# Optimization experiments

Measured on AMD Instinct MI355X. Metric: run time of the kernel, lower is better.

The kernel has to match this reference:

```python
import jax, jax.numpy as jnp
import numpy as np

N, D = 2, 256
M, L, K, DV = 8, 4, 4, 32
LK = L * K
LEVEL_HW = [(96, 96), (48, 48), (24, 24), (12, 12)]
S = sum(h * w for h, w in LEVEL_HW)  # 12240 flattened pyramid tokens
Q = S
OFFSET_SCALE = 0.5  # sampling_offset_scale_factor


def setup_inputs() -> dict:
    ks = jax.random.split(jax.random.key(0), 16)
    def lin(k, din, dout):
        return jax.random.normal(k, (din, dout), jnp.float32) / np.sqrt(din)
    return {
        "queries": jax.random.normal(ks[0], (N, Q, D), jnp.float32),
        "query_geometries": jax.random.uniform(ks[1], (N, Q, 4), jnp.float32, minval=0.1, maxval=0.9),
        "src_values": jax.random.normal(ks[2], (N, S, D), jnp.float32),
        "W_off": lin(ks[3], D, M * LK * 2) * 0.01,
        "b_off": jax.random.normal(ks[4], (M * LK * 2,), jnp.float32),
        "W_attn": lin(ks[5], D, M * LK),
        "b_attn": jnp.zeros((M * LK,), jnp.float32),
        "W_val": lin(ks[6], D, M * DV),
        "b_val": jnp.zeros((M * DV,), jnp.float32),
        "W_out": lin(ks[7], M * DV, D),
        "b_out": jnp.zeros((D,), jnp.float32),
    }


def _bilinear_sample(vmap_l, grid):
    # vmap_l: [B, dv, H, W]; grid: [B, Q, K, 2] in [-1, 1]
    # Matches F.grid_sample(mode='bilinear', align_corners=False, padding_mode='zeros')
    B, dv, H, W = vmap_l.shape
    x = (grid[..., 0] + 1.0) * (W / 2) - 0.5
    y = (grid[..., 1] + 1.0) * (H / 2) - 0.5
    x0 = jnp.floor(x)
    y0 = jnp.floor(y)
    wx = x - x0
    wy = y - y0
    x0i = x0.astype(jnp.int32)
    y0i = y0.astype(jnp.int32)
    vflat = vmap_l.reshape(B, dv, H * W)

    def corner(xi, yi, w):
        valid = (xi >= 0) & (xi < W) & (yi >= 0) & (yi < H)
        idx = jnp.clip(yi, 0, H - 1) * W + jnp.clip(xi, 0, W - 1)
        g = jax.vmap(lambda vf, i: vf[:, i])(vflat, idx)  # [B, dv, Q, K]
        return g * (w * valid)[:, None, :, :]

    return (corner(x0i, y0i, (1 - wx) * (1 - wy))
            + corner(x0i + 1, y0i, wx * (1 - wy))
            + corner(x0i, y0i + 1, (1 - wx) * wy)
            + corner(x0i + 1, y0i + 1, wx * wy))


def msdeform(queries, query_geometries, src_values, W_off, b_off, W_attn, b_attn,
             W_val, b_val, W_out, b_out):
    # attention weights: softmax over the L*K samples of each head
    attn = jax.nn.softmax((queries @ W_attn + b_attn).reshape(N, Q, M, LK), axis=-1)
    # predicted sampling offsets [N, Q, M, LK, 2]
    off = (queries @ W_off + b_off).reshape(N, Q, M, LK, 2)
    xy = query_geometries[..., :2]
    wh = query_geometries[..., 2:]
    scale = wh * (OFFSET_SCALE / K)  # wh * kv_count_per_level_inverse * sampling_offset_max_value
    pos = xy[:, :, None, None, :] + off * scale[:, :, None, None, :]  # normalized [0,1]
    # collapse (batch, head) -> B = N*M, rescale to [-1,1] for grid_sample semantics
    grid = (2.0 * pos - 1.0).transpose(0, 2, 1, 3, 4).reshape(N * M, Q, LK, 2)
    # project values and rebuild the per-level feature maps
    v = (src_values @ W_val + b_val).reshape(N, S, M, DV)
    samples, s = [], 0
    for l, (H, W) in enumerate(LEVEL_HW):
        vl = v[:, s:s + H * W].reshape(N, H, W, M, DV).transpose(0, 3, 4, 1, 2).reshape(N * M, DV, H, W)
        samples.append(_bilinear_sample(vl, grid[:, :, l * K:(l + 1) * K]))  # [N*M, DV, Q, K]
        s += H * W
    sampled = jnp.concatenate(samples, axis=-1)  # [N*M, DV, Q, LK]
    aw = attn.transpose(0, 2, 1, 3).reshape(N * M, 1, Q, LK)
    out = (sampled * aw).sum(-1)  # weighted reduction -> [N*M, DV, Q]
    out = out.reshape(N, M, DV, Q).transpose(0, 3, 1, 2).reshape(N, Q, M * DV)
    return out @ W_out + b_out  # backprojector


def reference(queries, query_geometries, src_values, W_off, b_off, W_attn, b_attn,
              W_val, b_val, W_out, b_out):
    return msdeform(queries, query_geometries, src_values, W_off, b_off, W_attn,
                    b_attn, W_val, b_val, W_out, b_out)
```

## Files before the change

kernel.cpp:

```cpp
#include <hip/hip_runtime.h>
#include <hip/hip_bf16.h>
#include <hip/hip_fp16.h>
#include <cstddef>

#define NB 2
#define QN 12240
#define SN 12240
#define MREAL 24480
#define MPAD  24576
#define MT    192

typedef unsigned short ushortT;
typedef unsigned int uintT;
typedef __bf16 bf16x8 __attribute__((ext_vector_type(8)));
typedef float f32x4 __attribute__((ext_vector_type(4)));
typedef float f32x2 __attribute__((ext_vector_type(2)));

__device__ __forceinline__ ushortT f2bf(float f) {
    uintT u = __float_as_uint(f);
    uintT r = u + 0x7fffu + ((u >> 16) & 1u);
    return (ushortT)(r >> 16);
}
__device__ __forceinline__ float bf_lo(uintT u) {
    return __uint_as_float(u << 16);
}
__device__ __forceinline__ float bf_hi(uintT u) {
    return __uint_as_float(u & 0xffff0000u);
}

__device__ __forceinline__ void async_ld16(const ushortT* g, ushortT* l) {
    __builtin_amdgcn_global_load_lds(
        (const __attribute__((address_space(1))) unsigned int*)g,
        (__attribute__((address_space(3))) unsigned int*)l, 16, 0, 0);
}

__global__ __launch_bounds__(256) void cast_all(
    const float* __restrict__ q, const float* __restrict__ src,
    const float* __restrict__ Wval, const float* __restrict__ Wattn,
    const float* __restrict__ Woff, const float* __restrict__ Wout,
    ushortT* __restrict__ qb, ushortT* __restrict__ sb,
    ushortT* __restrict__ tval, ushortT* __restrict__ tlo,
    ushortT* __restrict__ tout)
{
    int bx = blockIdx.x;
    if (bx < 6120) {
        const int issrc = bx >= 3060;
        const size_t idx = ((size_t)(bx - (issrc ? 3060 : 0)) * 256 + threadIdx.x) * 8;
        const float* in = issrc ? src : q;
        ushortT* out = issrc ? sb : qb;
        const float4 a = *(const float4*)(in + idx);
        const float4 b = *(const float4*)(in + idx + 4);
        uint4 o;
        o.x = (uintT)f2bf(a.x) | ((uintT)f2bf(a.y) << 16);
        o.y = (uintT)f2bf(a.z) | ((uintT)f2bf(a.w) << 16);
        o.z = (uintT)f2bf(b.x) | ((uintT)f2bf(b.y) << 16);
        o.w = (uintT)f2bf(b.z) | ((uintT)f2bf(b.w) << 16);
        *(uint4*)(out + idx) = o;
        return;
    }
    bx -= 6120;
    const float* W; ushortT* T; int n, Nw, trow;
    if (bx < 256)      { W = Wval;  T = tval; n = bx;       Nw = 256; trow = n; }
    else if (bx < 384) { W = Wattn; T = tlo;  n = bx - 256; Nw = 128; trow = n; }
    else if (bx < 640) { W = Woff;  T = tlo;  n = bx - 384; Nw = 256; trow = n + 128; }
    else               { W = Wout;  T = tout; n = bx - 640; Nw = 256; trow = n; }
    const int k = threadIdx.x;
    T[(size_t)trow * 256 + k] = f2bf(W[(size_t)k * Nw + n]);
}

__global__ __launch_bounds__(256) void gemm_vlo(
    const ushortT* __restrict__ q_bf, const ushortT* __restrict__ src_bf,
    const ushortT* __restrict__ wt_val, const ushortT* __restrict__ wt_lo,
    const float* __restrict__ b_val, const float* __restrict__ b_attn,
    const float* __restrict__ b_off,
    ushortT* __restrict__ v_bf, float* __restrict__ lo_ws)
{
    const int z = blockIdx.x >= 2;
    const int col0 = (z ? blockIdx.x - 2 : blockIdx.x) * 128;

    __shared__ __attribute__((aligned(16))) ushortT As[128 * 32];
    __shared__ __attribute__((aligned(16))) ushortT Bs[128 * 32];

    const ushortT* A  = z ? q_bf : src_bf;
    const ushortT* Bt = z ? wt_lo : wt_val;

    const int tid  = threadIdx.x;
    const int wave = tid >> 6;
    const int lane = tid & 63;
    const int row0 = blockIdx.y * 128;
    const int wr = (wave >> 1) * 64;
    const int wc = (wave & 1) * 64;

    f32x4 acc[4][4];
    #pragma unroll
    for (int i = 0; i < 4; i++)
        #pragma unroll
        for (int j = 0; j < 4; j++)
            acc[i][j] = (f32x4)0.f;

    const int srow = (lane >> 2);
    const int sk8  = (lane & 3) * 8;

    for (int k0 = 0; k0 < 256; k0 += 32) {
        #pragma unroll
        for (int j = 0; j < 2; j++) {
            const int r = wave * 32 + j * 16;
            async_ld16(A  + (size_t)(row0 + r + srow) * 256 + k0 + sk8, &As[r * 32]);
            async_ld16(Bt + (size_t)(col0 + r + srow) * 256 + k0 + sk8, &Bs[r * 32]);
        }
        __syncthreads();

        bf16x8 af[4], bfr[4];
        const int mrow = lane & 15;
        const int kq   = (lane >> 4) * 8;
        #pragma unroll
        for (int i = 0; i < 4; i++) {
            af[i]  = *(const bf16x8*)&As[(wr + i * 16 + mrow) * 32 + kq];
            bfr[i] = *(const bf16x8*)&Bs[(wc + i * 16 + mrow) * 32 + kq];
        }
        #pragma unroll
        for (int i = 0; i < 4; i++)
            #pragma unroll
            for (int j = 0; j < 4; j++)
                acc[i][j] = __builtin_amdgcn_mfma_f32_16x16x32_bf16(
                    af[i], bfr[j], acc[i][j], 0, 0, 0);
        __syncthreads();
    }

    const float* bp = z ? ((col0 < 128) ? b_attn : b_off) : b_val;
    const int cofs  = (z && col0 >= 128) ? 128 : 0;

    #pragma unroll
    for (int i = 0; i < 4; i++) {
        const int rbase = row0 + wr + i * 16 + ((lane >> 4) << 2);
        #pragma unroll
        for (int j = 0; j < 4; j++) {
            const int col = col0 + wc + j * 16 + (lane & 15);
            const float bb = bp[col - cofs];
            #pragma unroll
            for (int r = 0; r < 4; r++) {
                const int row = rbase + r;
                if (row < MREAL) {
                    const float val = acc[i][j][r] + bb;
                    if (z) {
                        lo_ws[(size_t)row * 384 + col] = val;
                    } else {
                        const int nn = row / SN;
                        const int s  = row - nn * SN;
                        const int head = col >> 5, ch = col & 31;
                        v_bf[(((size_t)nn * 8 + head) * SN + s) * 32 + ch] = f2bf(val);
                    }
                }
            }
        }
    }
}

__global__ __launch_bounds__(256) void gemm_out(
    const ushortT* __restrict__ A, const ushortT* __restrict__ Bt,
    const float* __restrict__ bias, float* __restrict__ C)
{
    __shared__ __attribute__((aligned(16))) ushortT As[128 * 32];
    __shared__ __attribute__((aligned(16))) ushortT Bs[128 * 32];

    const int tid  = threadIdx.x;
    const int wave = tid >> 6;
    const int lane = tid & 63;
    const int row0 = blockIdx.y * 128;
    const int col0 = blockIdx.x * 128;
    const int wr = (wave >> 1) * 64;
    const int wc = (wave & 1) * 64;

    f32x4 acc[4][4];
    #pragma unroll
    for (int i = 0; i < 4; i++)
        #pragma unroll
        for (int j = 0; j < 4; j++)
            acc[i][j] = (f32x4)0.f;

    const int srow = (lane >> 2);
    const int sk8  = (lane & 3) * 8;

    for (int k0 = 0; k0 < 256; k0 += 32) {
        #pragma unroll
        for (int j = 0; j < 2; j++) {
            const int r = wave * 32 + j * 16;
            async_ld16(A  + (size_t)(row0 + r + srow) * 256 + k0 + sk8, &As[r * 32]);
            async_ld16(Bt + (size_t)(col0 + r + srow) * 256 + k0 + sk8, &Bs[r * 32]);
        }
        __syncthreads();

        bf16x8 af[4], bfr[4];
        const int mrow = lane & 15;
        const int kq   = (lane >> 4) * 8;
        #pragma unroll
        for (int i = 0; i < 4; i++) {
            af[i]  = *(const bf16x8*)&As[(wr + i * 16 + mrow) * 32 + kq];
            bfr[i] = *(const bf16x8*)&Bs[(wc + i * 16 + mrow) * 32 + kq];
        }
        #pragma unroll
        for (int i = 0; i < 4; i++)
            #pragma unroll
            for (int j = 0; j < 4; j++)
                acc[i][j] = __builtin_amdgcn_mfma_f32_16x16x32_bf16(
                    af[i], bfr[j], acc[i][j], 0, 0, 0);
        __syncthreads();
    }

    #pragma unroll
    for (int i = 0; i < 4; i++) {
        const int rbase = row0 + wr + i * 16 + ((lane >> 4) << 2);
        #pragma unroll
        for (int j = 0; j < 4; j++) {
            const int col = col0 + wc + j * 16 + (lane & 15);
            const float bb = bias[col];
            #pragma unroll
            for (int r = 0; r < 4; r++) {
                const int row = rbase + r;
                if (row < MREAL)
                    C[(size_t)row * 256 + col] = acc[i][j][r] + bb;
            }
        }
    }
}

__global__ __launch_bounds__(128) void sample_kernel(
    const float* __restrict__ lo,
    const float* __restrict__ geom,
    const ushortT* __restrict__ v,
    ushortT* __restrict__ out)
{
    const int tid  = threadIdx.x;
    const int w    = tid >> 6;
    const int lane = tid & 63;
    const int qi   = lane >> 3;
    const int m    = blockIdx.y;
    const int n    = blockIdx.z;
    const int q    = blockIdx.x * 16 + w * 8 + qi;

    __shared__ __attribute__((aligned(16))) int pls[2][1568];

    const size_t qb = (size_t)n * QN + q;

    {
        const int p = lane & 7;
        const float* lorow = lo + qb * 384;
        const float2 lg = *(const float2*)(lorow + m * 16 + p * 2);
        const float4 of = *(const float4*)(lorow + 128 + m * 32 + p * 4);
        const float4 g  = *(const float4*)(geom + qb * 4);

        float mx = fmaxf(lg.x, lg.y);
        mx = fmaxf(mx, __shfl_xor(mx, 1));
        mx = fmaxf(mx, __shfl_xor(mx, 2));
        mx = fmaxf(mx, __shfl_xor(mx, 4));
        const float e0 = __expf(lg.x - mx);
        const float e1 = __expf(lg.y - mx);
        float s = e0 + e1;
        s += __shfl_xor(s, 1);
        s += __shfl_xor(s, 2);
        s += __shfl_xor(s, 4);
        const float inv = 1.f / s;

        const int l  = p >> 1;
        const int Wl = 96 >> l;
        const int s0 = (l == 0) ? 0 : (l == 1) ? 9216 : (l == 2) ? 11520 : 12096;
        const float cx = g.x, cy = g.y;
        const float sx = g.z * 0.125f, sy = g.w * 0.125f;
        int* myrec = &pls[w][qi * 196 + p * 24];

        #pragma unroll
        for (int t = 0; t < 2; t++) {
            const float ox = t ? of.z : of.x;
            const float oy = t ? of.w : of.y;
            const float wa = (t ? e1 : e0) * inv;

            const float x = (cx + ox * sx) * (float)Wl - 0.5f;
            const float y = (cy + oy * sy) * (float)Wl - 0.5f;
            const float xf = floorf(x), yf = floorf(y);
            const int x0 = (int)xf, y0 = (int)yf;
            const float wx = x - xf, wy = y - yf;

            const bool vx0 = (x0 >= 0) & (x0 < Wl);
            const bool vx1 = (x0 + 1 >= 0) & (x0 + 1 < Wl);
            const bool vy0 = (y0 >= 0) & (y0 < Wl);
            const bool vy1 = (y0 + 1 >= 0) & (y0 + 1 < Wl);

            const float w00 = (vx0 & vy0) ? wa * (1.f - wx) * (1.f - wy) : 0.f;
            const float w10 = (vx1 & vy0) ? wa * wx * (1.f - wy) : 0.f;
            const float w01 = (vx0 & vy1) ? wa * (1.f - wx) * wy : 0.f;
            const float w11 = (vx1 & vy1) ? wa * wx * wy : 0.f;

            const int xc0 = min(max(x0, 0), Wl - 1);
            const int xc1 = min(max(x0 + 1, 0), Wl - 1);
            const int yc0 = min(max(y0, 0), Wl - 1);
            const int yc1 = min(max(y0 + 1, 0), Wl - 1);

            const int o00 = (s0 + yc0 * Wl + xc0) << 6;
            const int dx  = (xc1 - xc0) << 6;
            const int dy  = ((yc1 - yc0) * Wl) << 6;

            int4 offs;
            offs.x = o00;
            offs.y = o00 + dx;
            offs.z = o00 + dy;
            offs.w = o00 + dy + dx;
            float4 wab, wcd;
            wab.x = w00; wab.y = w00; wab.z = w10; wab.w = w10;
            wcd.x = w01; wcd.y = w01; wcd.z = w11; wcd.w = w11;

            int* rp = myrec + t * 12;
            *(int4*)rp = offs;
            *(float4*)(rp + 4) = wab;
            *(float4*)(rp + 8) = wcd;
        }
    }
    __syncthreads();

    const int c  = lane & 7;
    const unsigned c8 = (unsigned)(c * 8);
    const unsigned char* vp = (const unsigned char*)
        (v + ((size_t)(n * 8 + m) * SN) * 32);
    const int* grec = &pls[w][qi * 196];

    f32x2 acc01 = (f32x2)0.f, acc23 = (f32x2)0.f;

    #pragma unroll
    for (int lk = 0; lk < 16; lk++) {
        const int* r = grec + lk * 12;
        const int4 offs = *(const int4*)r;
        const f32x2* wp = (const f32x2*)(r + 4);

        const uint2 u0 = *(const uint2*)(vp + ((unsigned)offs.x + c8));
        const uint2 u1 = *(const uint2*)(vp + ((unsigned)offs.y + c8));
        const uint2 u2 = *(const uint2*)(vp + ((unsigned)offs.z + c8));
        const uint2 u3 = *(const uint2*)(vp + ((unsigned)offs.w + c8));

        const f32x2 w0 = wp[0], w1 = wp[1], w2 = wp[2], w3 = wp[3];

        f32x2 t;
        t.x = bf_lo(u0.x); t.y = bf_hi(u0.x); acc01 += w0 * t;
        t.x = bf_lo(u0.y); t.y = bf_hi(u0.y); acc23 += w0 * t;
        t.x = bf_lo(u1.x); t.y = bf_hi(u1.x); acc01 += w1 * t;
        t.x = bf_lo(u1.y); t.y = bf_hi(u1.y); acc23 += w1 * t;
        t.x = bf_lo(u2.x); t.y = bf_hi(u2.x); acc01 += w2 * t;
        t.x = bf_lo(u2.y); t.y = bf_hi(u2.y); acc23 += w2 * t;
        t.x = bf_lo(u3.x); t.y = bf_hi(u3.x); acc01 += w3 * t;
        t.x = bf_lo(u3.y); t.y = bf_hi(u3.y); acc23 += w3 * t;
    }

    ushort4 o;
    o.x = f2bf(acc01.x); o.y = f2bf(acc01.y); o.z = f2bf(acc23.x); o.w = f2bf(acc23.y);
    *(ushort4*)(out + qb * 256 + m * 32 + c * 4) = o;
}

extern "C" void kernel_launch(void* const* d_in, const int* in_sizes, int n_in,
                              void* d_out, int out_size, void* d_ws, size_t ws_size,
                              hipStream_t stream)
{
    const float* queries = (const float*)d_in[0];
    const float* geom    = (const float*)d_in[1];
    const float* src     = (const float*)d_in[2];
    const float* W_off   = (const float*)d_in[3];
    const float* b_off   = (const float*)d_in[4];
    const float* W_attn  = (const float*)d_in[5];
    const float* b_attn  = (const float*)d_in[6];
    const float* W_val   = (const float*)d_in[7];
    const float* b_val   = (const float*)d_in[8];
    const float* W_out   = (const float*)d_in[9];
    const float* b_out   = (const float*)d_in[10];
    float* out = (float*)d_out;

    ushortT* wsb = (ushortT*)d_ws;
    const size_t PADROW = (size_t)MPAD * 256;
    ushortT* q_bf    = wsb;
    ushortT* srcmdv  = wsb + PADROW;
    ushortT* v_bf    = wsb + 2 * PADROW;
    ushortT* wt_val  = wsb + 3 * PADROW;
    ushortT* wt_lo   = wt_val + 65536;
    ushortT* wt_out  = wt_lo + 98304;
    float* lo_ws = (float*)(wt_out + 65536);

    dim3 blk(256);

    cast_all<<<dim3(7016), blk, 0, stream>>>(
        queries, src, W_val, W_attn, W_off, W_out,
        q_bf, srcmdv, wt_val, wt_lo, wt_out);

    gemm_vlo<<<dim3(5, MT), blk, 0, stream>>>(
        q_bf, srcmdv, wt_val, wt_lo, b_val, b_attn, b_off, v_bf, lo_ws);

    sample_kernel<<<dim3(QN / 16, 8, NB), dim3(128), 0, stream>>>(
        lo_ws, geom, v_bf, srcmdv);

    gemm_out<<<dim3(2, MT), blk, 0, stream>>>(srcmdv, wt_out, b_out, out);
}
```

Measured before the change: 208.2 us.

## Software-pipeline bilinear gathers in sample kernel and double block size

The 16-iteration gather loop in the sampling kernel becomes four explicit groups of 16 loads. Two groups are issued ahead of consumption, with sched_barrier fences keeping the compiler from collapsing the schedule, so more memory latency can overlap. Blocks grow from 2 to 4 waves (32 queries each), and the out-of-range queries in the last block are clamped to the final query, which rewrites the same values. Each query's sample records in shared memory are reordered so that the two samples per thread sit 8 records apart. This raises register pressure and shared-memory use per block, which may reduce occupancy.

```diff
diff --git a/kernel.cpp b/kernel.cpp
--- a/kernel.cpp
+++ b/kernel.cpp
@@ -224,7 +224,7 @@
     }
 }
 
-__global__ __launch_bounds__(128) void sample_kernel(
+__global__ __launch_bounds__(256) void sample_kernel(
     const float* __restrict__ lo,
     const float* __restrict__ geom,
     const ushortT* __restrict__ v,
@@ -236,9 +236,10 @@
     const int qi   = lane >> 3;
     const int m    = blockIdx.y;
     const int n    = blockIdx.z;
-    const int q    = blockIdx.x * 16 + w * 8 + qi;
-
-    __shared__ __attribute__((aligned(16))) int pls[2][1568];
+    int q = blockIdx.x * 32 + w * 8 + qi;
+    q = min(q, QN - 1);
+
+    __shared__ __attribute__((aligned(16))) int pls[4][1568];
 
     const size_t qb = (size_t)n * QN + q;
 
@@ -266,7 +267,7 @@
         const int s0 = (l == 0) ? 0 : (l == 1) ? 9216 : (l == 2) ? 11520 : 12096;
         const float cx = g.x, cy = g.y;
         const float sx = g.z * 0.125f, sy = g.w * 0.125f;
-        int* myrec = &pls[w][qi * 196 + p * 24];
+        int* myrec = &pls[w][qi * 196 + p * 12];
 
         #pragma unroll
         for (int t = 0; t < 2; t++) {
@@ -308,7 +309,7 @@
             wab.x = w00; wab.y = w00; wab.z = w10; wab.w = w10;
             wcd.x = w01; wcd.y = w01; wcd.z = w11; wcd.w = w11;
 
-            int* rp = myrec + t * 12;
+            int* rp = myrec + t * 96;
             *(int4*)rp = offs;
             *(float4*)(rp + 4) = wab;
             *(float4*)(rp + 8) = wcd;
@@ -324,29 +325,77 @@
 
     f32x2 acc01 = (f32x2)0.f, acc23 = (f32x2)0.f;
 
-    #pragma unroll
-    for (int lk = 0; lk < 16; lk++) {
-        const int* r = grec + lk * 12;
-        const int4 offs = *(const int4*)r;
-        const f32x2* wp = (const f32x2*)(r + 4);
-
-        const uint2 u0 = *(const uint2*)(vp + ((unsigned)offs.x + c8));
-        const uint2 u1 = *(const uint2*)(vp + ((unsigned)offs.y + c8));
-        const uint2 u2 = *(const uint2*)(vp + ((unsigned)offs.z + c8));
-        const uint2 u3 = *(const uint2*)(vp + ((unsigned)offs.w + c8));
-
-        const f32x2 w0 = wp[0], w1 = wp[1], w2 = wp[2], w3 = wp[3];
-
-        f32x2 t;
-        t.x = bf_lo(u0.x); t.y = bf_hi(u0.x); acc01 += w0 * t;
-        t.x = bf_lo(u0.y); t.y = bf_hi(u0.y); acc23 += w0 * t;
-        t.x = bf_lo(u1.x); t.y = bf_hi(u1.x); acc01 += w1 * t;
-        t.x = bf_lo(u1.y); t.y = bf_hi(u1.y); acc23 += w1 * t;
-        t.x = bf_lo(u2.x); t.y = bf_hi(u2.x); acc01 += w2 * t;
-        t.x = bf_lo(u2.y); t.y = bf_hi(u2.y); acc23 += w2 * t;
-        t.x = bf_lo(u3.x); t.y = bf_hi(u3.x); acc01 += w3 * t;
-        t.x = bf_lo(u3.y); t.y = bf_hi(u3.y); acc23 += w3 * t;
-    }
+#define GOFFS(G, O0,O1,O2,O3) \
+    const int4 O0 = *(const int4*)(grec + ((G)*4+0)*12); \
+    const int4 O1 = *(const int4*)(grec + ((G)*4+1)*12); \
+    const int4 O2 = *(const int4*)(grec + ((G)*4+2)*12); \
+    const int4 O3 = *(const int4*)(grec + ((G)*4+3)*12);
+
+#define GISSUE(O, U0,U1,U2,U3) \
+    const uint2 U0 = *(const uint2*)(vp + ((unsigned)(O).x + c8)); \
+    const uint2 U1 = *(const uint2*)(vp + ((unsigned)(O).y + c8)); \
+    const uint2 U2 = *(const uint2*)(vp + ((unsigned)(O).z + c8)); \
+    const uint2 U3 = *(const uint2*)(vp + ((unsigned)(O).w + c8));
+
+#define GCONSUME(G, R, U0,U1,U2,U3) { \
+    const f32x2* wp = (const f32x2*)(grec + ((G)*4+(R))*12 + 4); \
+    const f32x2 wA = wp[0], wB = wp[1], wC = wp[2], wD = wp[3]; \
+    f32x2 t; \
+    t.x = bf_lo(U0.x); t.y = bf_hi(U0.x); acc01 += wA * t; \
+    t.x = bf_lo(U0.y); t.y = bf_hi(U0.y); acc23 += wA * t; \
+    t.x = bf_lo(U1.x); t.y = bf_hi(U1.x); acc01 += wB * t; \
+    t.x = bf_lo(U1.y); t.y = bf_hi(U1.y); acc23 += wB * t; \
+    t.x = bf_lo(U2.x); t.y = bf_hi(U2.x); acc01 += wC * t; \
+    t.x = bf_lo(U2.y); t.y = bf_hi(U2.y); acc23 += wC * t; \
+    t.x = bf_lo(U3.x); t.y = bf_hi(U3.x); acc01 += wD * t; \
+    t.x = bf_lo(U3.y); t.y = bf_hi(U3.y); acc23 += wD * t; }
+
+    GOFFS(0, oa0,oa1,oa2,oa3)
+    GISSUE(oa0, a00,a01,a02,a03)
+    GISSUE(oa1, a10,a11,a12,a13)
+    GISSUE(oa2, a20,a21,a22,a23)
+    GISSUE(oa3, a30,a31,a32,a33)
+    GOFFS(1, ob0,ob1,ob2,ob3)
+    GISSUE(ob0, b00,b01,b02,b03)
+    GISSUE(ob1, b10,b11,b12,b13)
+    GISSUE(ob2, b20,b21,b22,b23)
+    GISSUE(ob3, b30,b31,b32,b33)
+    __builtin_amdgcn_sched_barrier(0);
+
+    GCONSUME(0,0, a00,a01,a02,a03)
+    GCONSUME(0,1, a10,a11,a12,a13)
+    GCONSUME(0,2, a20,a21,a22,a23)
+    GCONSUME(0,3, a30,a31,a32,a33)
+    GOFFS(2, oc0,oc1,oc2,oc3)
+    GISSUE(oc0, c00,c01,c02,c03)
+    GISSUE(oc1, c10,c11,c12,c13)
+    GISSUE(oc2, c20,c21,c22,c23)
+    GISSUE(oc3, c30,c31,c32,c33)
+    __builtin_amdgcn_sched_barrier(0);
+
+    GCONSUME(1,0, b00,b01,b02,b03)
+    GCONSUME(1,1, b10,b11,b12,b13)
+    GCONSUME(1,2, b20,b21,b22,b23)
+    GCONSUME(1,3, b30,b31,b32,b33)
+    GOFFS(3, od0,od1,od2,od3)
+    GISSUE(od0, d00,d01,d02,d03)
+    GISSUE(od1, d10,d11,d12,d13)
+    GISSUE(od2, d20,d21,d22,d23)
+    GISSUE(od3, d30,d31,d32,d33)
+    __builtin_amdgcn_sched_barrier(0);
+
+    GCONSUME(2,0, c00,c01,c02,c03)
+    GCONSUME(2,1, c10,c11,c12,c13)
+    GCONSUME(2,2, c20,c21,c22,c23)
+    GCONSUME(2,3, c30,c31,c32,c33)
+    GCONSUME(3,0, d00,d01,d02,d03)
+    GCONSUME(3,1, d10,d11,d12,d13)
+    GCONSUME(3,2, d20,d21,d22,d23)
+    GCONSUME(3,3, d30,d31,d32,d33)
+
+#undef GOFFS
+#undef GISSUE
+#undef GCONSUME
 
     ushort4 o;
     o.x = f2bf(acc01.x); o.y = f2bf(acc01.y); o.z = f2bf(acc23.x); o.w = f2bf(acc23.y);
@@ -389,7 +438,7 @@
     gemm_vlo<<<dim3(5, MT), blk, 0, stream>>>(
         q_bf, srcmdv, wt_val, wt_lo, b_val, b_attn, b_off, v_bf, lo_ws);
 
-    sample_kernel<<<dim3(QN / 16, 8, NB), dim3(128), 0, stream>>>(
+    sample_kernel<<<dim3((QN + 31) / 32, 8, NB), dim3(256), 0, stream>>>(
         lo_ws, geom, v_bf, srcmdv);
 
     gemm_out<<<dim3(2, MT), blk, 0, stream>>>(srcmdv, wt_out, b_out, out);
```

Result: no change. 207.1 us (-0.5%).

## Software-pipeline bilinear gathers with inline-asm loads and manual vmcnt waits

Applied to the files above, without the earlier changes.

The sampling kernel's gather loop is rewritten so the 64 corner loads are issued in groups of 16 through inline-asm global_load_dwordx2. Explicit s_waitcnt vmcnt waits and sched barriers make the consumption of one group overlap the next group's loads. The goal is to keep many gathers in flight and hide memory latency in this gather-bound stage. Blocks also grow from 128 to 256 threads, with a clamped query index to cover the ragged tail. The per-sample record layout in LDS is reordered. The inline-asm hazard handling relies on manual waits and costs extra VGPRs, which may reduce occupancy.

```diff
diff --git a/kernel.cpp b/kernel.cpp
--- a/kernel.cpp
+++ b/kernel.cpp
@@ -15,6 +15,7 @@
 typedef __bf16 bf16x8 __attribute__((ext_vector_type(8)));
 typedef float f32x4 __attribute__((ext_vector_type(4)));
 typedef float f32x2 __attribute__((ext_vector_type(2)));
+typedef unsigned u32x2v __attribute__((ext_vector_type(2)));
 
 __device__ __forceinline__ ushortT f2bf(float f) {
     uintT u = __float_as_uint(f);
@@ -32,6 +33,13 @@
     __builtin_amdgcn_global_load_lds(
         (const __attribute__((address_space(1))) unsigned int*)g,
         (__attribute__((address_space(3))) unsigned int*)l, 16, 0, 0);
+}
+
+__device__ __forceinline__ u32x2v gload8(const void* base, unsigned voff) {
+    u32x2v r;
+    asm volatile("global_load_dwordx2 %0, %1, %2"
+                 : "=v"(r) : "v"(voff), "s"(base));
+    return r;
 }
 
 __global__ __launch_bounds__(256) void cast_all(
@@ -224,7 +232,7 @@
     }
 }
 
-__global__ __launch_bounds__(128) void sample_kernel(
+__global__ __launch_bounds__(256) void sample_kernel(
     const float* __restrict__ lo,
     const float* __restrict__ geom,
     const ushortT* __restrict__ v,
@@ -236,9 +244,10 @@
     const int qi   = lane >> 3;
     const int m    = blockIdx.y;
     const int n    = blockIdx.z;
-    const int q    = blockIdx.x * 16 + w * 8 + qi;
-
-    __shared__ __attribute__((aligned(16))) int pls[2][1568];
+    int q = blockIdx.x * 32 + w * 8 + qi;
+    q = min(q, QN - 1);
+
+    __shared__ __attribute__((aligned(16))) int pls[4][1568];
 
     const size_t qb = (size_t)n * QN + q;
 
@@ -266,7 +275,7 @@
         const int s0 = (l == 0) ? 0 : (l == 1) ? 9216 : (l == 2) ? 11520 : 12096;
         const float cx = g.x, cy = g.y;
         const float sx = g.z * 0.125f, sy = g.w * 0.125f;
-        int* myrec = &pls[w][qi * 196 + p * 24];
+        int* myrec = &pls[w][qi * 196 + p * 12];
 
         #pragma unroll
         for (int t = 0; t < 2; t++) {
@@ -308,7 +317,7 @@
             wab.x = w00; wab.y = w00; wab.z = w10; wab.w = w10;
             wcd.x = w01; wcd.y = w01; wcd.z = w11; wcd.w = w11;
 
-            int* rp = myrec + t * 12;
+            int* rp = myrec + t * 96;
             *(int4*)rp = offs;
             *(float4*)(rp + 4) = wab;
             *(float4*)(rp + 8) = wcd;
@@ -324,29 +333,89 @@
 
     f32x2 acc01 = (f32x2)0.f, acc23 = (f32x2)0.f;
 
-    #pragma unroll
-    for (int lk = 0; lk < 16; lk++) {
-        const int* r = grec + lk * 12;
-        const int4 offs = *(const int4*)r;
-        const f32x2* wp = (const f32x2*)(r + 4);
-
-        const uint2 u0 = *(const uint2*)(vp + ((unsigned)offs.x + c8));
-        const uint2 u1 = *(const uint2*)(vp + ((unsigned)offs.y + c8));
-        const uint2 u2 = *(const uint2*)(vp + ((unsigned)offs.z + c8));
-        const uint2 u3 = *(const uint2*)(vp + ((unsigned)offs.w + c8));
-
-        const f32x2 w0 = wp[0], w1 = wp[1], w2 = wp[2], w3 = wp[3];
-
-        f32x2 t;
-        t.x = bf_lo(u0.x); t.y = bf_hi(u0.x); acc01 += w0 * t;
-        t.x = bf_lo(u0.y); t.y = bf_hi(u0.y); acc23 += w0 * t;
-        t.x = bf_lo(u1.x); t.y = bf_hi(u1.x); acc01 += w1 * t;
-        t.x = bf_lo(u1.y); t.y = bf_hi(u1.y); acc23 += w1 * t;
-        t.x = bf_lo(u2.x); t.y = bf_hi(u2.x); acc01 += w2 * t;
-        t.x = bf_lo(u2.y); t.y = bf_hi(u2.y); acc23 += w2 * t;
-        t.x = bf_lo(u3.x); t.y = bf_hi(u3.x); acc01 += w3 * t;
-        t.x = bf_lo(u3.y); t.y = bf_hi(u3.y); acc23 += w3 * t;
-    }
+#define GISSUE(O, U0,U1,U2,U3) \
+    u32x2v U0 = gload8(vp, (unsigned)(O).x + c8); \
+    u32x2v U1 = gload8(vp, (unsigned)(O).y + c8); \
+    u32x2v U2 = gload8(vp, (unsigned)(O).z + c8); \
+    u32x2v U3 = gload8(vp, (unsigned)(O).w + c8);
+
+#define GCONS(IDX, U0,U1,U2,U3) { \
+    const f32x2* wp = (const f32x2*)(grec + (IDX)*12 + 4); \
+    const f32x2 wA = wp[0], wB = wp[1], wC = wp[2], wD = wp[3]; \
+    f32x2 t; \
+    t.x = bf_lo(U0.x); t.y = bf_hi(U0.x); acc01 += wA * t; \
+    t.x = bf_lo(U0.y); t.y = bf_hi(U0.y); acc23 += wA * t; \
+    t.x = bf_lo(U1.x); t.y = bf_hi(U1.x); acc01 += wB * t; \
+    t.x = bf_lo(U1.y); t.y = bf_hi(U1.y); acc23 += wB * t; \
+    t.x = bf_lo(U2.x); t.y = bf_hi(U2.x); acc01 += wC * t; \
+    t.x = bf_lo(U2.y); t.y = bf_hi(U2.y); acc23 += wC * t; \
+    t.x = bf_lo(U3.x); t.y = bf_hi(U3.x); acc01 += wD * t; \
+    t.x = bf_lo(U3.y); t.y = bf_hi(U3.y); acc23 += wD * t; }
+
+#define VMWAIT16 asm volatile("s_waitcnt vmcnt(16)"); __builtin_amdgcn_sched_barrier(0);
+#define VMWAIT0  asm volatile("s_waitcnt vmcnt(0)");  __builtin_amdgcn_sched_barrier(0);
+
+    const int4 oa0 = *(const int4*)(grec + 0 * 12);
+    const int4 oa1 = *(const int4*)(grec + 1 * 12);
+    const int4 oa2 = *(const int4*)(grec + 2 * 12);
+    const int4 oa3 = *(const int4*)(grec + 3 * 12);
+    GISSUE(oa0, a0u,a1u,a2u,a3u)
+    GISSUE(oa1, b0u,b1u,b2u,b3u)
+    GISSUE(oa2, c0u,c1u,c2u,c3u)
+    GISSUE(oa3, d0u,d1u,d2u,d3u)
+    const int4 ob0 = *(const int4*)(grec + 4 * 12);
+    const int4 ob1 = *(const int4*)(grec + 5 * 12);
+    const int4 ob2 = *(const int4*)(grec + 6 * 12);
+    const int4 ob3 = *(const int4*)(grec + 7 * 12);
+    GISSUE(ob0, e0u,e1u,e2u,e3u)
+    GISSUE(ob1, f0u,f1u,f2u,f3u)
+    GISSUE(ob2, g0u,g1u,g2u,g3u)
+    GISSUE(ob3, h0u,h1u,h2u,h3u)
+
+    VMWAIT16
+    GCONS(0, a0u,a1u,a2u,a3u)
+    GCONS(1, b0u,b1u,b2u,b3u)
+    GCONS(2, c0u,c1u,c2u,c3u)
+    GCONS(3, d0u,d1u,d2u,d3u)
+    const int4 oc0 = *(const int4*)(grec + 8 * 12);
+    const int4 oc1 = *(const int4*)(grec + 9 * 12);
+    const int4 oc2 = *(const int4*)(grec + 10 * 12);
+    const int4 oc3 = *(const int4*)(grec + 11 * 12);
+    GISSUE(oc0, i0u,i1u,i2u,i3u)
+    GISSUE(oc1, j0u,j1u,j2u,j3u)
+    GISSUE(oc2, k0u,k1u,k2u,k3u)
+    GISSUE(oc3, l0u,l1u,l2u,l3u)
+
+    VMWAIT16
+    GCONS(4, e0u,e1u,e2u,e3u)
+    GCONS(5, f0u,f1u,f2u,f3u)
+    GCONS(6, g0u,g1u,g2u,g3u)
+    GCONS(7, h0u,h1u,h2u,h3u)
+    const int4 od0 = *(const int4*)(grec + 12 * 12);
+    const int4 od1 = *(const int4*)(grec + 13 * 12);
+    const int4 od2 = *(const int4*)(grec + 14 * 12);
+    const int4 od3 = *(const int4*)(grec + 15 * 12);
+    GISSUE(od0, p0u,p1u,p2u,p3u)
+    GISSUE(od1, q0u,q1u,q2u,q3u)
+    GISSUE(od2, r0u,r1u,r2u,r3u)
+    GISSUE(od3, s0u,s1u,s2u,s3u)
+
+    VMWAIT16
+    GCONS(8,  i0u,i1u,i2u,i3u)
+    GCONS(9,  j0u,j1u,j2u,j3u)
+    GCONS(10, k0u,k1u,k2u,k3u)
+    GCONS(11, l0u,l1u,l2u,l3u)
+
+    VMWAIT0
+    GCONS(12, p0u,p1u,p2u,p3u)
+    GCONS(13, q0u,q1u,q2u,q3u)
+    GCONS(14, r0u,r1u,r2u,r3u)
+    GCONS(15, s0u,s1u,s2u,s3u)
+
+#undef GISSUE
+#undef GCONS
+#undef VMWAIT16
+#undef VMWAIT0
 
     ushort4 o;
     o.x = f2bf(acc01.x); o.y = f2bf(acc01.y); o.z = f2bf(acc23.x); o.w = f2bf(acc23.y);
@@ -389,7 +458,7 @@
     gemm_vlo<<<dim3(5, MT), blk, 0, stream>>>(
         q_bf, srcmdv, wt_val, wt_lo, b_val, b_attn, b_off, v_bf, lo_ws);
 
-    sample_kernel<<<dim3(QN / 16, 8, NB), dim3(128), 0, stream>>>(
+    sample_kernel<<<dim3((QN + 31) / 32, 8, NB), dim3(256), 0, stream>>>(
         lo_ws, geom, v_bf, srcmdv);
 
     gemm_out<<<dim3(2, MT), blk, 0, stream>>>(srcmdv, wt_out, b_out, out);
```

New measurement: 206.3 us. Within noise of the previous version (-0.9%).
